# Kernel optimization log

Measured on AMD Instinct MI355X. Metric: run time of the kernel, lower is better.

Reference implementation:

```python
import jax, jax.numpy as jnp
import numpy as np

N_NODES = 100000


def _add_self_loops(edge_index, n):
    loop = jnp.arange(n, dtype=edge_index.dtype)
    src = jnp.concatenate([edge_index[0], loop])
    dst = jnp.concatenate([edge_index[1], loop])
    return src, dst


def _gcn_norm(src, dst, n):
    # PyG gcn_norm: degree over dst (col), norm = d^-1/2[src] * d^-1/2[dst]
    deg = jax.ops.segment_sum(jnp.ones_like(dst, dtype=jnp.float32), dst, num_segments=n)
    dinv = jnp.where(deg > 0, jax.lax.rsqrt(jnp.maximum(deg, 1.0)), 0.0)
    return dinv[src] * dinv[dst]


def _gcn_conv(x, W, b, src, dst, norm, n):
    h = x @ W                              # [N, out]
    msg = h[src] * norm[:, None]           # gather + scale  [E', out]
    out = jax.ops.segment_sum(msg, dst, num_segments=n)  # scatter-add
    if b is not None:
        out = out + b
    return out


def setup_inputs() -> dict:
    key = jax.random.key(0)
    ks = jax.random.split(key, 8)
    n, e = N_NODES, 1600000
    in_d, hid, out_d, L = 128, 64, 64, 3
    x = jax.random.normal(ks[0], (n, in_d), dtype=jnp.float32)
    edge_index = jax.random.randint(ks[1], (2, e), 0, n, dtype=jnp.int64)
    s = lambda fan_in: 1.0 / np.sqrt(fan_in)
    W_in = jax.random.normal(ks[2], (in_d, hid), dtype=jnp.float32) * s(in_d)
    b_in = jnp.zeros((hid,), dtype=jnp.float32)
    W_h = jax.random.normal(ks[3], (L, hid, hid), dtype=jnp.float32) * s(hid)
    b_h = jnp.zeros((L, hid), dtype=jnp.float32)
    W_out = jax.random.normal(ks[4], (hid, out_d), dtype=jnp.float32) * s(hid)
    return {"x": x, "edge_index": edge_index, "W_in": W_in, "b_in": b_in,
            "W_h": W_h, "b_h": b_h, "W_out": W_out}


def reference(x, edge_index, W_in, b_in, W_h, b_h, W_out):
    n = x.shape[0]
    src, dst = _add_self_loops(edge_index, n)
    norm = _gcn_norm(src, dst, n)
    h = _gcn_conv(x, W_in, b_in, src, dst, norm, n)
    for i in range(W_h.shape[0]):
        h = _gcn_conv(h, W_h[i], b_h[i], src, dst, norm, n)
        h = jax.nn.relu(h)
    return _gcn_conv(h, W_out, None, src, dst, norm, n)
```

## Files before the change

kernel.cpp:

```cpp
#include <hip/hip_runtime.h>
#include <hip/hip_fp16.h>

#define HID 64
#define BIN_SHIFT 9
#define BIN_SIZE  512
#define SC_TILE   8192


__global__ void zero_i(int* __restrict__ p, int n) {
    int i = blockIdx.x * 256 + threadIdx.x, st = gridDim.x * 256;
    for (; i < n; i += st) p[i] = 0;
}

__global__ void dinv_k(const int* __restrict__ deg, float* __restrict__ dinv, int N) {
    int i = blockIdx.x * 256 + threadIdx.x;
    if (i < N) dinv[i] = rsqrtf((float)deg[i] + 1.0f);
}

__global__ void bin_count(const int* __restrict__ dst, int* __restrict__ binCount,
                          int E, int nbins) {
    __shared__ int c[1024];
    for (int i = threadIdx.x; i < nbins; i += 256) c[i] = 0;
    __syncthreads();
    int chunk = (E + gridDim.x - 1) / gridDim.x;
    int s0 = blockIdx.x * chunk, s1 = min(E, s0 + chunk);
    for (int e = s0 + threadIdx.x; e < s1; e += 256)
        atomicAdd(&c[dst[e] >> BIN_SHIFT], 1);
    __syncthreads();
    for (int i = threadIdx.x; i < nbins; i += 256)
        if (c[i]) atomicAdd(&binCount[i], c[i]);
}

__global__ void bin_scan(const int* __restrict__ binCount, int* __restrict__ binOff,
                         int* __restrict__ binCursor, int nb, int E) {
    __shared__ int s[256];
    int t = threadIdx.x, base = t * 4;
    int v0 = 0, v1 = 0, v2 = 0, v3 = 0;
    if (base + 0 < nb) v0 = binCount[base + 0];
    if (base + 1 < nb) v1 = binCount[base + 1];
    if (base + 2 < nb) v2 = binCount[base + 2];
    if (base + 3 < nb) v3 = binCount[base + 3];
    int sum = v0 + v1 + v2 + v3;
    s[t] = sum; __syncthreads();
    for (int off = 1; off < 256; off <<= 1) {
        int x = (t >= off) ? s[t - off] : 0;
        __syncthreads(); s[t] += x; __syncthreads();
    }
    int run = s[t] - sum;
    if (base + 0 < nb) { binOff[base + 0] = run; binCursor[base + 0] = run; } run += v0;
    if (base + 1 < nb) { binOff[base + 1] = run; binCursor[base + 1] = run; } run += v1;
    if (base + 2 < nb) { binOff[base + 2] = run; binCursor[base + 2] = run; } run += v2;
    if (base + 3 < nb) { binOff[base + 3] = run; binCursor[base + 3] = run; } run += v3;
    if (t == 0) binOff[nb] = E;
}

__global__ void bin_scatter(const int* __restrict__ src, const int* __restrict__ dst,
                            int* __restrict__ binCursor, unsigned* __restrict__ packed,
                            int E, int nbins) {
    __shared__ int cnt[1024];
    __shared__ int cur[1024];
    int t = threadIdx.x;
    int s0 = blockIdx.x * SC_TILE, s1 = min(E, s0 + SC_TILE);
    for (int i = t; i < nbins; i += 256) cnt[i] = 0;
    __syncthreads();
    for (int e = s0 + t; e < s1; e += 256)
        atomicAdd(&cnt[dst[e] >> BIN_SHIFT], 1);
    __syncthreads();
    for (int b = t; b < nbins; b += 256)
        cur[b] = cnt[b] ? atomicAdd(&binCursor[b], cnt[b]) : 0;
    __syncthreads();
    for (int e = s0 + t; e < s1; e += 256) {
        int d = dst[e];
        int b = d >> BIN_SHIFT;
        int pos = atomicAdd(&cur[b], 1);
        packed[pos] = ((unsigned)src[e] << BIN_SHIFT) | (unsigned)(d & (BIN_SIZE - 1));
    }
}

__global__ void csr_count(const unsigned* __restrict__ packed, const int* __restrict__ binOff,
                          int* __restrict__ deg, int N) {
    __shared__ int c[BIN_SIZE];
    int t = threadIdx.x, b = blockIdx.x;
    for (int i = t; i < BIN_SIZE; i += 256) c[i] = 0;
    int j0 = binOff[b], j1 = binOff[b + 1];
    __syncthreads();
    for (int j = j0 + t; j < j1; j += 256)
        atomicAdd(&c[packed[j] & (BIN_SIZE - 1)], 1);
    __syncthreads();
    int base = b << BIN_SHIFT;
    for (int i = t; i < BIN_SIZE; i += 256) {
        int nd = base + i;
        if (nd < N) deg[nd] = c[i];
    }
}

__global__ void csr_scatter(const unsigned* __restrict__ packed, const int* __restrict__ binOff,
                            const int* __restrict__ rp, int* __restrict__ esrc, int N) {
    __shared__ int cur[BIN_SIZE];
    __shared__ int rps[BIN_SIZE];
    int t = threadIdx.x, b = blockIdx.x;
    int base = b << BIN_SHIFT;
    for (int i = t; i < BIN_SIZE; i += 256) {
        cur[i] = 0;
        int nd = base + i;
        rps[i] = (nd < N) ? rp[nd] : 0;
    }
    int j0 = binOff[b], j1 = binOff[b + 1];
    __syncthreads();
    for (int j = j0 + t; j < j1; j += 256) {
        unsigned p = packed[j];
        int dl = p & (BIN_SIZE - 1);
        int pos = rps[dl] + atomicAdd(&cur[dl], 1);
        esrc[pos] = (int)(p >> BIN_SHIFT);
    }
}

__global__ void scan1(const int* __restrict__ in, int* __restrict__ out,
                      int* __restrict__ bsum, int n) {
    __shared__ int s[256];
    int t = threadIdx.x, base = blockIdx.x * 1024 + t * 4;
    int v0 = 0, v1 = 0, v2 = 0, v3 = 0;
    if (base + 0 < n) v0 = in[base + 0];
    if (base + 1 < n) v1 = in[base + 1];
    if (base + 2 < n) v2 = in[base + 2];
    if (base + 3 < n) v3 = in[base + 3];
    int sum = v0 + v1 + v2 + v3;
    s[t] = sum; __syncthreads();
    for (int off = 1; off < 256; off <<= 1) {
        int x = (t >= off) ? s[t - off] : 0;
        __syncthreads(); s[t] += x; __syncthreads();
    }
    if (t == 255) bsum[blockIdx.x] = s[255];
    int run = s[t] - sum;
    if (base + 0 < n) out[base + 0] = run; run += v0;
    if (base + 1 < n) out[base + 1] = run; run += v1;
    if (base + 2 < n) out[base + 2] = run; run += v2;
    if (base + 3 < n) out[base + 3] = run;
}

__global__ void scan2(int* __restrict__ bsum, int nb) {
    __shared__ int s[256];
    int t = threadIdx.x, base = t * 4;
    int v0 = 0, v1 = 0, v2 = 0, v3 = 0;
    if (base + 0 < nb) v0 = bsum[base + 0];
    if (base + 1 < nb) v1 = bsum[base + 1];
    if (base + 2 < nb) v2 = bsum[base + 2];
    if (base + 3 < nb) v3 = bsum[base + 3];
    int sum = v0 + v1 + v2 + v3;
    s[t] = sum; __syncthreads();
    for (int off = 1; off < 256; off <<= 1) {
        int x = (t >= off) ? s[t - off] : 0;
        __syncthreads(); s[t] += x; __syncthreads();
    }
    int run = s[t] - sum;
    if (base + 0 < nb) bsum[base + 0] = run; run += v0;
    if (base + 1 < nb) bsum[base + 1] = run; run += v1;
    if (base + 2 < nb) bsum[base + 2] = run; run += v2;
    if (base + 3 < nb) bsum[base + 3] = run;
}

__global__ void scan3(int* __restrict__ out, const int* __restrict__ bsum,
                      int n, int N, int E) {
    int i = blockIdx.x * 256 + threadIdx.x;
    if (i < n) out[i] += bsum[i >> 10];
    if (i == 0) out[N] = E;
}

#define HSTRIDE 132
__global__ __launch_bounds__(256, 3)
void gemm_tile(const float* __restrict__ H, const float* __restrict__ W,
               const float* __restrict__ dinv, __half* __restrict__ out,
               int N, int K) {
    __shared__ float h_s[64 * HSTRIDE];
    __shared__ float w_s[64 * 64];
    int tid  = threadIdx.x;
    int col4 = tid & 15;
    int row0 = (tid >> 4) * 8;
    int n0   = blockIdx.x * 128;
    float4 acc[8];
    #pragma unroll
    for (int r = 0; r < 8; ++r) acc[r] = make_float4(0.f, 0.f, 0.f, 0.f);

    int nchunk = K >> 6;
    for (int kc = 0; kc < nchunk; ++kc) {
        __syncthreads();
        #pragma unroll
        for (int m = 0; m < 8; ++m) {
            int i  = tid + m * 256;
            int r  = i >> 4;
            int k0 = (i & 15) * 4;
            int nd = n0 + r;
            float4 v = make_float4(0.f, 0.f, 0.f, 0.f);
            if (nd < N) v = *(const float4*)&H[(size_t)nd * K + kc * 64 + k0];
            h_s[(k0 + 0) * HSTRIDE + r] = v.x;
            h_s[(k0 + 1) * HSTRIDE + r] = v.y;
            h_s[(k0 + 2) * HSTRIDE + r] = v.z;
            h_s[(k0 + 3) * HSTRIDE + r] = v.w;
        }
        #pragma unroll
        for (int m = 0; m < 4; ++m) {
            int i = tid + m * 256;
            *(float4*)&w_s[i * 4] = *(const float4*)&W[(size_t)(kc * 64) * HID + i * 4];
        }
        __syncthreads();
        #pragma unroll 8
        for (int k = 0; k < 64; ++k) {
            float4 w  = *(const float4*)&w_s[k * 64 + col4 * 4];
            float4 hA = *(const float4*)&h_s[k * HSTRIDE + row0];
            float4 hB = *(const float4*)&h_s[k * HSTRIDE + row0 + 4];
            acc[0].x = fmaf(hA.x, w.x, acc[0].x); acc[0].y = fmaf(hA.x, w.y, acc[0].y);
            acc[0].z = fmaf(hA.x, w.z, acc[0].z); acc[0].w = fmaf(hA.x, w.w, acc[0].w);
            acc[1].x = fmaf(hA.y, w.x, acc[1].x); acc[1].y = fmaf(hA.y, w.y, acc[1].y);
            acc[1].z = fmaf(hA.y, w.z, acc[1].z); acc[1].w = fmaf(hA.y, w.w, acc[1].w);
            acc[2].x = fmaf(hA.z, w.x, acc[2].x); acc[2].y = fmaf(hA.z, w.y, acc[2].y);
            acc[2].z = fmaf(hA.z, w.z, acc[2].z); acc[2].w = fmaf(hA.z, w.w, acc[2].w);
            acc[3].x = fmaf(hA.w, w.x, acc[3].x); acc[3].y = fmaf(hA.w, w.y, acc[3].y);
            acc[3].z = fmaf(hA.w, w.z, acc[3].z); acc[3].w = fmaf(hA.w, w.w, acc[3].w);
            acc[4].x = fmaf(hB.x, w.x, acc[4].x); acc[4].y = fmaf(hB.x, w.y, acc[4].y);
            acc[4].z = fmaf(hB.x, w.z, acc[4].z); acc[4].w = fmaf(hB.x, w.w, acc[4].w);
            acc[5].x = fmaf(hB.y, w.x, acc[5].x); acc[5].y = fmaf(hB.y, w.y, acc[5].y);
            acc[5].z = fmaf(hB.y, w.z, acc[5].z); acc[5].w = fmaf(hB.y, w.w, acc[5].w);
            acc[6].x = fmaf(hB.z, w.x, acc[6].x); acc[6].y = fmaf(hB.z, w.y, acc[6].y);
            acc[6].z = fmaf(hB.z, w.z, acc[6].z); acc[6].w = fmaf(hB.z, w.w, acc[6].w);
            acc[7].x = fmaf(hB.w, w.x, acc[7].x); acc[7].y = fmaf(hB.w, w.y, acc[7].y);
            acc[7].z = fmaf(hB.w, w.z, acc[7].z); acc[7].w = fmaf(hB.w, w.w, acc[7].w);
        }
    }
    int nd0 = n0 + row0;
    #pragma unroll
    for (int r = 0; r < 8; ++r) {
        int nd = nd0 + r;
        if (nd < N) {
            float dv = dinv[nd];
            __half2* o = (__half2*)&out[(size_t)nd * HID + col4 * 4];
            o[0] = __halves2half2(__float2half_rn(acc[r].x * dv), __float2half_rn(acc[r].y * dv));
            o[1] = __halves2half2(__float2half_rn(acc[r].z * dv), __float2half_rn(acc[r].w * dv));
        }
    }
}

__global__ void agg_csr(const __half* __restrict__ tmp, const int* __restrict__ rp,
                        const int* __restrict__ esrc, const float* __restrict__ dinv,
                        const float* __restrict__ bias, float* __restrict__ out,
                        int N, int do_relu) {
    int wave = threadIdx.x >> 6;
    int lane = threadIdx.x & 63;
    int g    = lane & 7;
    int sub  = lane >> 3;
    for (int d = blockIdx.x * 4 + wave; d < N; d += gridDim.x * 4) {
        float acc[8];
        #pragma unroll
        for (int i = 0; i < 8; ++i) acc[i] = 0.0f;
        if (sub == 0) {
            uint4 v = ((const uint4*)(tmp + (size_t)d * HID))[g];
            const __half2* h2 = (const __half2*)&v;
            #pragma unroll
            for (int i = 0; i < 4; ++i) {
                float2 f = __half22float2(h2[i]);
                acc[2 * i]     = f.x;
                acc[2 * i + 1] = f.y;
            }
        }
        int j0 = rp[d], j1 = rp[d + 1];
        for (int base = j0; base < j1; base += 64) {
            int cnt = min(64, j1 - base);
            int sp = (lane < cnt) ? esrc[base + lane] : 0;
            int jj = 0;
            for (; jj + 8 < cnt; jj += 16) {
                int e0 = jj + sub;
                int e1 = jj + 8 + sub;
                int s0 = __shfl(sp, e0);
                int s1 = __shfl(sp, e1 & 63);
                bool v1ok = e1 < cnt;
                uint4 v0 = ((const uint4*)(tmp + (size_t)s0 * HID))[g];
                uint4 v1 = make_uint4(0, 0, 0, 0);
                if (v1ok) v1 = ((const uint4*)(tmp + (size_t)s1 * HID))[g];
                const __half2* h0 = (const __half2*)&v0;
                #pragma unroll
                for (int i = 0; i < 4; ++i) {
                    float2 f = __half22float2(h0[i]);
                    acc[2 * i] += f.x; acc[2 * i + 1] += f.y;
                }
                if (v1ok) {
                    const __half2* h1 = (const __half2*)&v1;
                    #pragma unroll
                    for (int i = 0; i < 4; ++i) {
                        float2 f = __half22float2(h1[i]);
                        acc[2 * i] += f.x; acc[2 * i + 1] += f.y;
                    }
                }
            }
            for (; jj < cnt; jj += 8) {
                int e = jj + sub;
                int s = __shfl(sp, min(e, cnt - 1));
                if (e < cnt) {
                    uint4 v = ((const uint4*)(tmp + (size_t)s * HID))[g];
                    const __half2* h2 = (const __half2*)&v;
                    #pragma unroll
                    for (int i = 0; i < 4; ++i) {
                        float2 f = __half22float2(h2[i]);
                        acc[2 * i] += f.x; acc[2 * i + 1] += f.y;
                    }
                }
            }
        }
        #pragma unroll
        for (int i = 0; i < 8; ++i) {
            float a = acc[i];
            a += __shfl_xor(a, 8);
            a += __shfl_xor(a, 16);
            a += __shfl_xor(a, 32);
            acc[i] = a;
        }
        if (sub == 0) {
            float di = dinv[d];
            float4 o0, o1;
            o0.x = di * acc[0]; o0.y = di * acc[1];
            o0.z = di * acc[2]; o0.w = di * acc[3];
            o1.x = di * acc[4]; o1.y = di * acc[5];
            o1.z = di * acc[6]; o1.w = di * acc[7];
            if (bias != nullptr) {
                const float4* bp = (const float4*)&bias[g * 8];
                float4 b0 = bp[0], b1 = bp[1];
                o0.x += b0.x; o0.y += b0.y; o0.z += b0.z; o0.w += b0.w;
                o1.x += b1.x; o1.y += b1.y; o1.z += b1.z; o1.w += b1.w;
            }
            if (do_relu) {
                o0.x = fmaxf(o0.x, 0.f); o0.y = fmaxf(o0.y, 0.f);
                o0.z = fmaxf(o0.z, 0.f); o0.w = fmaxf(o0.w, 0.f);
                o1.x = fmaxf(o1.x, 0.f); o1.y = fmaxf(o1.y, 0.f);
                o1.z = fmaxf(o1.z, 0.f); o1.w = fmaxf(o1.w, 0.f);
            }
            float* orow = &out[(size_t)d * HID + g * 8];
            *(float4*)orow       = o0;
            *(float4*)(orow + 4) = o1;
        }
    }
}

extern "C" void kernel_launch(void* const* d_in, const int* in_sizes, int n_in,
                              void* d_out, int out_size, void* d_ws, size_t ws_size,
                              hipStream_t stream) {
    const float* x     = (const float*)d_in[0];
    const int*   ei    = (const int*)d_in[1];
    const float* W_in  = (const float*)d_in[2];
    const float* b_in  = (const float*)d_in[3];
    const float* W_h   = (const float*)d_in[4];
    const float* b_h   = (const float*)d_in[5];
    const float* W_out = (const float*)d_in[6];

    const int K0 = in_sizes[2] / HID;
    const int N  = in_sizes[0] / K0;
    const int E  = in_sizes[1] / 2;
    const int* srcp = ei;
    const int* dstp = ei + E;

    const int NH = N * HID;
    const size_t Npad = ((size_t)N + 255) & ~(size_t)255;
    const int nbins = (N + BIN_SIZE - 1) >> BIN_SHIFT;

    float* ACC = (float*)d_out;

    float*    dinv   = (float*)d_ws;
    __half*   tmp    = (__half*)(dinv + Npad);
    unsigned* packed = (unsigned*)tmp;
    int*      degi   = (int*)(tmp + NH);
    int*      rp     = degi + Npad;
    int*      bsum   = rp + Npad + 256;
    int*      esrc   = bsum + 1024;
    int*      binCount  = esrc + E;
    int*      binOff    = binCount + 1024;
    int*      binCursor = binOff + 1026;

    const int tgrid = (N + 127) / 128;
    const int agrid = 2048;
    const int nb    = (N + 1023) / 1024;
    const int sgrid = (E + SC_TILE - 1) / SC_TILE;

    zero_i<<<1, 256, 0, stream>>>(binCount, nbins);
    bin_count<<<nbins, 256, 0, stream>>>(dstp, binCount, E, nbins);
    bin_scan<<<1, 256, 0, stream>>>(binCount, binOff, binCursor, nbins, E);
    bin_scatter<<<sgrid, 256, 0, stream>>>(srcp, dstp, binCursor, packed, E, nbins);
    csr_count<<<nbins, 256, 0, stream>>>(packed, binOff, degi, N);
    dinv_k<<<(N + 255) / 256, 256, 0, stream>>>(degi, dinv, N);
    scan1<<<nb, 256, 0, stream>>>(degi, rp, bsum, N);
    scan2<<<1, 256, 0, stream>>>(bsum, nb);
    scan3<<<(N + 255) / 256, 256, 0, stream>>>(rp, bsum, N, N, E);
    csr_scatter<<<nbins, 256, 0, stream>>>(packed, binOff, rp, esrc, N);

    gemm_tile<<<tgrid, 256, 0, stream>>>(x, W_in, dinv, tmp, N, 128);
    agg_csr<<<agrid, 256, 0, stream>>>(tmp, rp, esrc, dinv, b_in, ACC, N, 0);
    for (int l = 0; l < 3; ++l) {
        gemm_tile<<<tgrid, 256, 0, stream>>>(ACC, W_h + (size_t)l * HID * HID, dinv, tmp, N, 64);
        agg_csr<<<agrid, 256, 0, stream>>>(tmp, rp, esrc, dinv, b_h + (size_t)l * HID, ACC, N, 1);
    }
    gemm_tile<<<tgrid, 256, 0, stream>>>(ACC, W_out, dinv, tmp, N, 64);
    agg_csr<<<agrid, 256, 0, stream>>>(tmp, rp, esrc, dinv, nullptr, ACC, N, 0);
}
```

Baseline: 525.7 us.

## Replace FP32 SIMT GEMM with MFMA fp16 GEMM and store intermediate activations in fp16

```diff
diff --git a/kernel.cpp b/kernel.cpp
--- a/kernel.cpp
+++ b/kernel.cpp
@@ -7,6 +7,9 @@
 #define SC_TILE   8192
 
 
+typedef _Float16 f16x8 __attribute__((ext_vector_type(8)));
+typedef float    f32x4 __attribute__((ext_vector_type(4)));
+
 __global__ void zero_i(int* __restrict__ p, int n) {
     int i = blockIdx.x * 256 + threadIdx.x, st = gridDim.x * 256;
     for (; i < n; i += st) p[i] = 0;
@@ -15,6 +18,100 @@
 __global__ void dinv_k(const int* __restrict__ deg, float* __restrict__ dinv, int N) {
     int i = blockIdx.x * 256 + threadIdx.x;
     if (i < N) dinv[i] = rsqrtf((float)deg[i] + 1.0f);
+}
+
+__global__ void wfrag_prep(const float* __restrict__ W_in, const float* __restrict__ W_h,
+                           const float* __restrict__ W_out, __half* __restrict__ wfrag) {
+    int s = blockIdx.x, l = threadIdx.x;
+    const float* W; int base, ls;
+    if (s < 16)      { W = W_in;                      base = 0;                ls = s; }
+    else if (s < 40) { int t = s - 16; int L = t >> 3;
+                       W = W_h + (size_t)L * 64 * 64; base = 1024 + L * 512;   ls = t & 7; }
+    else             { W = W_out;                     base = 2560;             ls = s - 40; }
+    int ks = ls >> 2, ct = ls & 3;
+    int col = ct * 16 + (l & 15);
+    int k0  = ks * 32 + (l >> 4) * 8;
+    __half v[8];
+    #pragma unroll
+    for (int j = 0; j < 8; ++j) v[j] = __float2half_rn(W[(size_t)(k0 + j) * HID + col]);
+    *(uint4*)&wfrag[(size_t)(base + ls * 64 + l) * 8] = *(uint4*)v;
+}
+
+template<bool IN32, int NKS>
+__global__ __launch_bounds__(256)
+void gemm_mfma(const void* __restrict__ Hin, const __half* __restrict__ wfl,
+               const float* __restrict__ dinv, __half* __restrict__ out, int N) {
+    const int l  = threadIdx.x & 63;
+    const int wv = threadIdx.x >> 6;
+    const int rA = l & 15;
+    const int gK = l >> 4;
+    const int rb = blockIdx.x * 128 + wv * 32;
+
+    f16x8 bf[NKS][4];
+    #pragma unroll
+    for (int ks = 0; ks < NKS; ++ks)
+        #pragma unroll
+        for (int ct = 0; ct < 4; ++ct)
+            bf[ks][ct] = *(const f16x8*)(wfl + (size_t)((ks * 4 + ct) * 64 + l) * 8);
+
+    f16x8 af[NKS][2];
+    #pragma unroll
+    for (int rt = 0; rt < 2; ++rt) {
+        int r = rb + rt * 16 + rA; if (r > N - 1) r = N - 1;
+        if (IN32) {
+            const float* H = (const float*)Hin;
+            const float* p = H + (size_t)r * (NKS * 32) + gK * 8;
+            #pragma unroll
+            for (int ks = 0; ks < NKS; ++ks) {
+                f32x4 a = *(const f32x4*)(p + ks * 32);
+                f32x4 b = *(const f32x4*)(p + ks * 32 + 4);
+                f16x8 t;
+                t[0] = (_Float16)a[0]; t[1] = (_Float16)a[1];
+                t[2] = (_Float16)a[2]; t[3] = (_Float16)a[3];
+                t[4] = (_Float16)b[0]; t[5] = (_Float16)b[1];
+                t[6] = (_Float16)b[2]; t[7] = (_Float16)b[3];
+                af[ks][rt] = t;
+            }
+        } else {
+            const __half* H = (const __half*)Hin;
+            #pragma unroll
+            for (int ks = 0; ks < NKS; ++ks)
+                af[ks][rt] = *(const f16x8*)(H + (size_t)r * HID + ks * 32 + gK * 8);
+        }
+    }
+
+    f32x4 acc[2][4];
+    #pragma unroll
+    for (int rt = 0; rt < 2; ++rt)
+        #pragma unroll
+        for (int ct = 0; ct < 4; ++ct)
+            acc[rt][ct] = (f32x4){0.f, 0.f, 0.f, 0.f};
+
+    #pragma unroll
+    for (int ks = 0; ks < NKS; ++ks)
+        #pragma unroll
+        for (int rt = 0; rt < 2; ++rt)
+            #pragma unroll
+            for (int ct = 0; ct < 4; ++ct)
+                acc[rt][ct] = __builtin_amdgcn_mfma_f32_16x16x32_f16(
+                    af[ks][rt], bf[ks][ct], acc[rt][ct], 0, 0, 0);
+
+    #pragma unroll
+    for (int rt = 0; rt < 2; ++rt) {
+        int r0 = rb + rt * 16 + gK * 4;
+        float dv[4];
+        #pragma unroll
+        for (int j = 0; j < 4; ++j) dv[j] = dinv[min(r0 + j, N - 1)];
+        #pragma unroll
+        for (int ct = 0; ct < 4; ++ct)
+            #pragma unroll
+            for (int j = 0; j < 4; ++j) {
+                int r = r0 + j;
+                if (r < N)
+                    out[(size_t)r * HID + ct * 16 + rA] =
+                        __float2half_rn(acc[rt][ct][j] * dv[j]);
+            }
+    }
 }
 
 __global__ void bin_count(const int* __restrict__ dst, int* __restrict__ binCount,
@@ -166,83 +263,10 @@
     if (i == 0) out[N] = E;
 }
 
-#define HSTRIDE 132
-__global__ __launch_bounds__(256, 3)
-void gemm_tile(const float* __restrict__ H, const float* __restrict__ W,
-               const float* __restrict__ dinv, __half* __restrict__ out,
-               int N, int K) {
-    __shared__ float h_s[64 * HSTRIDE];
-    __shared__ float w_s[64 * 64];
-    int tid  = threadIdx.x;
-    int col4 = tid & 15;
-    int row0 = (tid >> 4) * 8;
-    int n0   = blockIdx.x * 128;
-    float4 acc[8];
-    #pragma unroll
-    for (int r = 0; r < 8; ++r) acc[r] = make_float4(0.f, 0.f, 0.f, 0.f);
-
-    int nchunk = K >> 6;
-    for (int kc = 0; kc < nchunk; ++kc) {
-        __syncthreads();
-        #pragma unroll
-        for (int m = 0; m < 8; ++m) {
-            int i  = tid + m * 256;
-            int r  = i >> 4;
-            int k0 = (i & 15) * 4;
-            int nd = n0 + r;
-            float4 v = make_float4(0.f, 0.f, 0.f, 0.f);
-            if (nd < N) v = *(const float4*)&H[(size_t)nd * K + kc * 64 + k0];
-            h_s[(k0 + 0) * HSTRIDE + r] = v.x;
-            h_s[(k0 + 1) * HSTRIDE + r] = v.y;
-            h_s[(k0 + 2) * HSTRIDE + r] = v.z;
-            h_s[(k0 + 3) * HSTRIDE + r] = v.w;
-        }
-        #pragma unroll
-        for (int m = 0; m < 4; ++m) {
-            int i = tid + m * 256;
-            *(float4*)&w_s[i * 4] = *(const float4*)&W[(size_t)(kc * 64) * HID + i * 4];
-        }
-        __syncthreads();
-        #pragma unroll 8
-        for (int k = 0; k < 64; ++k) {
-            float4 w  = *(const float4*)&w_s[k * 64 + col4 * 4];
-            float4 hA = *(const float4*)&h_s[k * HSTRIDE + row0];
-            float4 hB = *(const float4*)&h_s[k * HSTRIDE + row0 + 4];
-            acc[0].x = fmaf(hA.x, w.x, acc[0].x); acc[0].y = fmaf(hA.x, w.y, acc[0].y);
-            acc[0].z = fmaf(hA.x, w.z, acc[0].z); acc[0].w = fmaf(hA.x, w.w, acc[0].w);
-            acc[1].x = fmaf(hA.y, w.x, acc[1].x); acc[1].y = fmaf(hA.y, w.y, acc[1].y);
-            acc[1].z = fmaf(hA.y, w.z, acc[1].z); acc[1].w = fmaf(hA.y, w.w, acc[1].w);
-            acc[2].x = fmaf(hA.z, w.x, acc[2].x); acc[2].y = fmaf(hA.z, w.y, acc[2].y);
-            acc[2].z = fmaf(hA.z, w.z, acc[2].z); acc[2].w = fmaf(hA.z, w.w, acc[2].w);
-            acc[3].x = fmaf(hA.w, w.x, acc[3].x); acc[3].y = fmaf(hA.w, w.y, acc[3].y);
-            acc[3].z = fmaf(hA.w, w.z, acc[3].z); acc[3].w = fmaf(hA.w, w.w, acc[3].w);
-            acc[4].x = fmaf(hB.x, w.x, acc[4].x); acc[4].y = fmaf(hB.x, w.y, acc[4].y);
-            acc[4].z = fmaf(hB.x, w.z, acc[4].z); acc[4].w = fmaf(hB.x, w.w, acc[4].w);
-            acc[5].x = fmaf(hB.y, w.x, acc[5].x); acc[5].y = fmaf(hB.y, w.y, acc[5].y);
-            acc[5].z = fmaf(hB.y, w.z, acc[5].z); acc[5].w = fmaf(hB.y, w.w, acc[5].w);
-            acc[6].x = fmaf(hB.z, w.x, acc[6].x); acc[6].y = fmaf(hB.z, w.y, acc[6].y);
-            acc[6].z = fmaf(hB.z, w.z, acc[6].z); acc[6].w = fmaf(hB.z, w.w, acc[6].w);
-            acc[7].x = fmaf(hB.w, w.x, acc[7].x); acc[7].y = fmaf(hB.w, w.y, acc[7].y);
-            acc[7].z = fmaf(hB.w, w.z, acc[7].z); acc[7].w = fmaf(hB.w, w.w, acc[7].w);
-        }
-    }
-    int nd0 = n0 + row0;
-    #pragma unroll
-    for (int r = 0; r < 8; ++r) {
-        int nd = nd0 + r;
-        if (nd < N) {
-            float dv = dinv[nd];
-            __half2* o = (__half2*)&out[(size_t)nd * HID + col4 * 4];
-            o[0] = __halves2half2(__float2half_rn(acc[r].x * dv), __float2half_rn(acc[r].y * dv));
-            o[1] = __halves2half2(__float2half_rn(acc[r].z * dv), __float2half_rn(acc[r].w * dv));
-        }
-    }
-}
-
 __global__ void agg_csr(const __half* __restrict__ tmp, const int* __restrict__ rp,
                         const int* __restrict__ esrc, const float* __restrict__ dinv,
-                        const float* __restrict__ bias, float* __restrict__ out,
-                        int N, int do_relu) {
+                        const float* __restrict__ bias, float* __restrict__ outf,
+                        __half* __restrict__ houtp, int N, int do_relu) {
     int wave = threadIdx.x >> 6;
     int lane = threadIdx.x & 63;
     int g    = lane & 7;
@@ -314,26 +338,29 @@
         }
         if (sub == 0) {
             float di = dinv[d];
-            float4 o0, o1;
-            o0.x = di * acc[0]; o0.y = di * acc[1];
-            o0.z = di * acc[2]; o0.w = di * acc[3];
-            o1.x = di * acc[4]; o1.y = di * acc[5];
-            o1.z = di * acc[6]; o1.w = di * acc[7];
+            float o[8];
+            #pragma unroll
+            for (int i = 0; i < 8; ++i) o[i] = di * acc[i];
             if (bias != nullptr) {
-                const float4* bp = (const float4*)&bias[g * 8];
-                float4 b0 = bp[0], b1 = bp[1];
-                o0.x += b0.x; o0.y += b0.y; o0.z += b0.z; o0.w += b0.w;
-                o1.x += b1.x; o1.y += b1.y; o1.z += b1.z; o1.w += b1.w;
+                #pragma unroll
+                for (int i = 0; i < 8; ++i) o[i] += bias[g * 8 + i];
             }
             if (do_relu) {
-                o0.x = fmaxf(o0.x, 0.f); o0.y = fmaxf(o0.y, 0.f);
-                o0.z = fmaxf(o0.z, 0.f); o0.w = fmaxf(o0.w, 0.f);
-                o1.x = fmaxf(o1.x, 0.f); o1.y = fmaxf(o1.y, 0.f);
-                o1.z = fmaxf(o1.z, 0.f); o1.w = fmaxf(o1.w, 0.f);
-            }
-            float* orow = &out[(size_t)d * HID + g * 8];
-            *(float4*)orow       = o0;
-            *(float4*)(orow + 4) = o1;
+                #pragma unroll
+                for (int i = 0; i < 8; ++i) o[i] = fmaxf(o[i], 0.0f);
+            }
+            if (houtp != nullptr) {
+                __half2 ph[4];
+                #pragma unroll
+                for (int i = 0; i < 4; ++i)
+                    ph[i] = __halves2half2(__float2half_rn(o[2 * i]),
+                                           __float2half_rn(o[2 * i + 1]));
+                *(uint4*)&houtp[(size_t)d * HID + g * 8] = *(uint4*)ph;
+            } else {
+                float* orow = &outf[(size_t)d * HID + g * 8];
+                *(float4*)orow       = make_float4(o[0], o[1], o[2], o[3]);
+                *(float4*)(orow + 4) = make_float4(o[4], o[5], o[6], o[7]);
+            }
         }
     }
 }
@@ -359,7 +386,8 @@
     const size_t Npad = ((size_t)N + 255) & ~(size_t)255;
     const int nbins = (N + BIN_SIZE - 1) >> BIN_SHIFT;
 
-    float* ACC = (float*)d_out;
+    float*  ACC = (float*)d_out;
+    __half* h16 = (__half*)d_out;
 
     float*    dinv   = (float*)d_ws;
     __half*   tmp    = (__half*)(dinv + Npad);
@@ -371,12 +399,16 @@
     int*      binCount  = esrc + E;
     int*      binOff    = binCount + 1024;
     int*      binCursor = binOff + 1026;
+    uintptr_t wf_addr = (uintptr_t)(binCursor + 1024);
+    wf_addr = (wf_addr + 15) & ~(uintptr_t)15;
+    __half*   wfrag  = (__half*)wf_addr;
 
     const int tgrid = (N + 127) / 128;
     const int agrid = 2048;
     const int nb    = (N + 1023) / 1024;
     const int sgrid = (E + SC_TILE - 1) / SC_TILE;
 
+    wfrag_prep<<<48, 64, 0, stream>>>(W_in, W_h, W_out, wfrag);
     zero_i<<<1, 256, 0, stream>>>(binCount, nbins);
     bin_count<<<nbins, 256, 0, stream>>>(dstp, binCount, E, nbins);
     bin_scan<<<1, 256, 0, stream>>>(binCount, binOff, binCursor, nbins, E);
@@ -388,12 +420,15 @@
     scan3<<<(N + 255) / 256, 256, 0, stream>>>(rp, bsum, N, N, E);
     csr_scatter<<<nbins, 256, 0, stream>>>(packed, binOff, rp, esrc, N);
 
-    gemm_tile<<<tgrid, 256, 0, stream>>>(x, W_in, dinv, tmp, N, 128);
-    agg_csr<<<agrid, 256, 0, stream>>>(tmp, rp, esrc, dinv, b_in, ACC, N, 0);
+    gemm_mfma<true, 4><<<tgrid, 256, 0, stream>>>(x, wfrag, dinv, tmp, N);
+    agg_csr<<<agrid, 256, 0, stream>>>(tmp, rp, esrc, dinv, b_in, nullptr, h16, N, 0);
     for (int l = 0; l < 3; ++l) {
-        gemm_tile<<<tgrid, 256, 0, stream>>>(ACC, W_h + (size_t)l * HID * HID, dinv, tmp, N, 64);
-        agg_csr<<<agrid, 256, 0, stream>>>(tmp, rp, esrc, dinv, b_h + (size_t)l * HID, ACC, N, 1);
-    }
-    gemm_tile<<<tgrid, 256, 0, stream>>>(ACC, W_out, dinv, tmp, N, 64);
-    agg_csr<<<agrid, 256, 0, stream>>>(tmp, rp, esrc, dinv, nullptr, ACC, N, 0);
-}
+        gemm_mfma<false, 2><<<tgrid, 256, 0, stream>>>(
+            h16, wfrag + (size_t)(1024 + l * 512) * 8, dinv, tmp, N);
+        agg_csr<<<agrid, 256, 0, stream>>>(tmp, rp, esrc, dinv, b_h + (size_t)l * HID,
+                                           nullptr, h16, N, 1);
+    }
+    gemm_mfma<false, 2><<<tgrid, 256, 0, stream>>>(
+        h16, wfrag + (size_t)2560 * 8, dinv, tmp, N);
+    agg_csr<<<agrid, 256, 0, stream>>>(tmp, rp, esrc, dinv, nullptr, ACC, nullptr, N, 0);
+}
```

Result: faster. 462.7 us (-12.0%).
